# Optimization experiments

Measured on AMD Instinct MI355X. Metric: run time of the kernel, lower is better.

## Reference

```python
import jax, jax.numpy as jnp
import numpy as np

T_SCHEDULE = 999.0
LOG_2PI = float(np.log(2.0 * np.pi))


def setup_inputs() -> dict:
    key = jax.random.key(0)
    k1, k2, k3 = jax.random.split(key, 3)
    xt = jax.random.normal(k1, (128, 3, 32, 32), dtype=jnp.float32)
    # integer-style diffusion timesteps in [0, 900); divided by t_schedule=999 inside
    t = jax.random.uniform(k2, (128,), dtype=jnp.float32) * 900.0
    gt_images = jax.random.normal(k3, (20000, 3, 32, 32), dtype=jnp.float32)
    return {"xt": xt, "t": t, "gt_images": gt_images}


def reference(xt, t, gt_images):
    # AnalyticFlow.forward_fast
    B = xt.shape[0]
    N = gt_images.shape[0]
    x = jax.lax.stop_gradient(xt.reshape(B, -1))  # original detaches x
    gt = gt_images.reshape(N, -1)                 # [N, D]
    D = x.shape[-1]
    tt = t / T_SCHEDULE                           # [B]
    sig = 1.0 - tt                                # [B]
    # log N(term_2; 0, I) summed over D, where term_2 = (x - t*gt)/(1-t).
    # ||x - t*gt||^2 = ||x||^2 - 2 t x.gt + t^2 ||gt||^2  (avoids B*N*D tensor)
    x2 = jnp.sum(x * x, axis=-1)                  # [B]
    g2 = jnp.sum(gt * gt, axis=-1)                # [N]
    xg = x @ gt.T                                 # [B, N] GEMM
    sq = x2[:, None] - 2.0 * tt[:, None] * xg + (tt * tt)[:, None] * g2[None, :]
    log_p = -0.5 * sq / (sig * sig)[:, None] - 0.5 * D * LOG_2PI  # [B, N]
    log_p = log_p - jnp.max(log_p)                # global-max shift as in original
    eta = jax.nn.softmax(log_p, axis=1)           # [B, N], rows sum to 1
    # drift = mean_n (N*eta_n) * (gt_n - x)/(1-t) = (eta @ gt - x)/(1-t)
    drift = (eta @ gt - x) / sig[:, None]         # [B, D]
    return drift.reshape(xt.shape)
```

## Files before the change

kernel.cpp:

```cpp
#include <hip/hip_runtime.h>
#include <stdint.h>

#define B_SZ   128
#define D_SZ   3072
#define N_SZ   20000
#define NPAD   20480

typedef __attribute__((ext_vector_type(8))) short  short8;
typedef __attribute__((ext_vector_type(4))) float  f32x4;

__device__ __forceinline__ unsigned short f2bf(float f) {
    unsigned u = __float_as_uint(f);
    u += 0x7FFFu + ((u >> 16) & 1u);
    return (unsigned short)(u >> 16);
}
__device__ __forceinline__ float bf2f(unsigned short h) {
    return __uint_as_float(((unsigned)h) << 16);
}
__device__ __forceinline__ unsigned fkey_enc(float f) {
    unsigned b = __float_as_uint(f);
    return (b & 0x80000000u) ? ~b : (b | 0x80000000u);
}
__device__ __forceinline__ float fkey_dec(unsigned u) {
    return __uint_as_float((u & 0x80000000u) ? (u ^ 0x80000000u) : ~u);
}

__device__ __forceinline__ void gl_lds16(const void* g, void* l) {
    __builtin_amdgcn_global_load_lds(
        (const __attribute__((address_space(1))) void*)g,
        (__attribute__((address_space(3))) void*)l, 16, 0, 0);
}

__global__ __launch_bounds__(256) void zero_ws(float* __restrict__ p)
{
    p[blockIdx.x * 256 + threadIdx.x] = 0.f;
}

__global__ __launch_bounds__(256) void prep_x(const float* __restrict__ x,
                                              unsigned short* __restrict__ xhi,
                                              unsigned short* __restrict__ xlo)
{
    int i = blockIdx.x * 256 + threadIdx.x;
    float v = x[i];
    unsigned short h = f2bf(v);
    xhi[i] = h;
    xlo[i] = f2bf(v - bf2f(h));
}

__global__ __launch_bounds__(256) void scores_kernel(
        const float* __restrict__ gt,
        const unsigned short* __restrict__ xhi,
        const unsigned short* __restrict__ xlo,
        float* __restrict__ XG,
        float* __restrict__ G2)
{
    __shared__ __align__(16) unsigned short Xhi_t[128 * 32];
    __shared__ __align__(16) unsigned short Xlo_t[128 * 32];
    __shared__ __align__(16) unsigned short Ghi_t[64 * 32];
    __shared__ __align__(16) unsigned short Glo_t[64 * 32];

    const int tid   = threadIdx.x;
    const int kc    = blockIdx.x & 7;
    const int nt    = blockIdx.x >> 3;
    const int nbase = nt * 64;
    const int kcb   = kc * 384;

    const int lane = tid & 63;
    const int wave = tid >> 6;
    const int mh = wave & 1;
    const int nh = wave >> 1;
    const int lm = lane & 15;
    const int qd = lane >> 4;

    const int gn = tid >> 2;
    const int gq = tid & 3;
    const int ng0 = nbase + gn;
    int grow = ng0 > N_SZ - 1 ? N_SZ - 1 : ng0;
    const float* gp0 = gt + (size_t)grow * D_SZ + kcb + gq * 8;

    float g2acc = 0.0f;

    f32x4 acc[4][2];
    #pragma unroll
    for (int i = 0; i < 4; i++)
        #pragma unroll
        for (int j = 0; j < 2; j++)
            acc[i][j] = (f32x4){0.f, 0.f, 0.f, 0.f};

    for (int k0 = 0; k0 < 384; k0 += 32) {
        #pragma unroll
        for (int i = 0; i < 2; i++) {
            int o  = (i * 256 + tid) * 16;
            int r  = o >> 6;
            int ke = (o & 63) >> 1;
            gl_lds16(xhi + (size_t)r * D_SZ + kcb + k0 + ke, (char*)Xhi_t + o);
            gl_lds16(xlo + (size_t)r * D_SZ + kcb + k0 + ke, (char*)Xlo_t + o);
        }
        f32x4 v0 = *(const f32x4*)(gp0 + k0);
        f32x4 v1 = *(const f32x4*)(gp0 + k0 + 4);
        short8 h8, l8;
        #pragma unroll
        for (int j = 0; j < 4; j++) {
            float a = v0[j], b = v1[j];
            unsigned short ha = f2bf(a), hb = f2bf(b);
            h8[j]     = (short)ha;  h8[j + 4] = (short)hb;
            l8[j]     = (short)f2bf(a - bf2f(ha));
            l8[j + 4] = (short)f2bf(b - bf2f(hb));
            g2acc += a * a + b * b;
        }
        *(short8*)&Ghi_t[gn * 32 + gq * 8] = h8;
        *(short8*)&Glo_t[gn * 32 + gq * 8] = l8;

        __syncthreads();

        short8 bhi[2], blo[2];
        #pragma unroll
        for (int ni = 0; ni < 2; ni++) {
            int r = nh * 32 + ni * 16 + lm;
            bhi[ni] = *(short8*)&Ghi_t[r * 32 + qd * 8];
            blo[ni] = *(short8*)&Glo_t[r * 32 + qd * 8];
        }
        #pragma unroll
        for (int mi = 0; mi < 4; mi++) {
            int r = mh * 64 + mi * 16 + lm;
            short8 ahi = *(short8*)&Xhi_t[r * 32 + qd * 8];
            short8 alo = *(short8*)&Xlo_t[r * 32 + qd * 8];
            #pragma unroll
            for (int ni = 0; ni < 2; ni++) {
                acc[mi][ni] = __builtin_amdgcn_mfma_f32_16x16x32_bf16(ahi, bhi[ni], acc[mi][ni], 0, 0, 0);
                acc[mi][ni] = __builtin_amdgcn_mfma_f32_16x16x32_bf16(ahi, blo[ni], acc[mi][ni], 0, 0, 0);
                acc[mi][ni] = __builtin_amdgcn_mfma_f32_16x16x32_bf16(alo, bhi[ni], acc[mi][ni], 0, 0, 0);
            }
        }
        __syncthreads();
    }

    g2acc += __shfl_xor(g2acc, 1);
    g2acc += __shfl_xor(g2acc, 2);
    if (gq == 0 && ng0 < N_SZ) atomicAdd(&G2[ng0], g2acc);

    #pragma unroll
    for (int mi = 0; mi < 4; mi++) {
        #pragma unroll
        for (int ni = 0; ni < 2; ni++) {
            int ncol = nh * 32 + ni * 16 + lm;
            int ng = nbase + ncol;
            if (ng < N_SZ) {
                #pragma unroll
                for (int i = 0; i < 4; i++) {
                    int m = mh * 64 + mi * 16 + qd * 4 + i;
                    atomicAdd(&XG[(size_t)m * NPAD + ng], acc[mi][ni][i]);
                }
            }
        }
    }
}

__global__ __launch_bounds__(256) void maxk(
        const float* __restrict__ XG, const float* __restrict__ G2,
        const float* __restrict__ tarr, unsigned* __restrict__ Mkey)
{
    const int b  = blockIdx.x >> 3;
    const int ch = blockIdx.x & 7;
    const int tid = threadIdx.x;
    float tt  = tarr[b] / 999.0f;
    float sig = 1.0f - tt;
    float inv = 1.0f / (sig * sig);
    float c1 = tt * inv, c2 = 0.5f * tt * tt * inv;
    const float* xg = XG + (size_t)b * NPAD;
    __shared__ float wred[4];

    float mx = -3.402823466e+38f;
    int n0 = ch * 2560;
    for (int n = n0 + tid; n < n0 + 2560; n += 256)
        if (n < N_SZ) mx = fmaxf(mx, c1 * xg[n] - c2 * G2[n]);
    #pragma unroll
    for (int o = 32; o > 0; o >>= 1) mx = fmaxf(mx, __shfl_xor(mx, o));
    if ((tid & 63) == 0) wred[tid >> 6] = mx;
    __syncthreads();
    if (tid == 0) {
        mx = fmaxf(fmaxf(wred[0], wred[1]), fmaxf(wred[2], wred[3]));
        atomicMax(&Mkey[b], fkey_enc(mx));
    }
}

__global__ __launch_bounds__(256) void expk(
        const float* __restrict__ XG, const float* __restrict__ G2,
        const float* __restrict__ tarr, const unsigned* __restrict__ Mkey,
        unsigned short* __restrict__ P, float* __restrict__ L)
{
    const int b  = blockIdx.x >> 3;
    const int ch = blockIdx.x & 7;
    const int tid = threadIdx.x;
    float tt  = tarr[b] / 999.0f;
    float sig = 1.0f - tt;
    float inv = 1.0f / (sig * sig);
    float c1 = tt * inv, c2 = 0.5f * tt * tt * inv;
    float m = fkey_dec(Mkey[b]);
    const float* xg = XG + (size_t)b * NPAD;
    unsigned short* prow = P + (size_t)b * NPAD;
    __shared__ float wred[4];

    float sum = 0.f;
    int n0 = ch * 2560;
    for (int n = n0 + tid; n < n0 + 2560; n += 256) {
        float p = 0.f;
        if (n < N_SZ) { p = expf(c1 * xg[n] - c2 * G2[n] - m); sum += p; }
        prow[n] = f2bf(p);
    }
    #pragma unroll
    for (int o = 32; o > 0; o >>= 1) sum += __shfl_xor(sum, o);
    if ((tid & 63) == 0) wred[tid >> 6] = sum;
    __syncthreads();
    if (tid == 0) atomicAdd(&L[b], wred[0] + wred[1] + wred[2] + wred[3]);
}

__global__ __launch_bounds__(256) void drift_kernel(
        const float* __restrict__ gt,
        const unsigned short* __restrict__ P,
        float* __restrict__ Dacc)
{
    __shared__ __align__(16) unsigned short Pt[128 * 32];
    __shared__ __align__(16) unsigned short Gt[128 * 40];

    const int tid = threadIdx.x;
    const int nt = blockIdx.x % 24;
    const int kc = blockIdx.x / 24;
    const int dbase = nt * 128;

    const int lane = tid & 63;
    const int wave = tid >> 6;
    const int mh = wave & 1;
    const int dh = wave >> 1;
    const int lm = lane & 15;
    const int qd = lane >> 4;

    const int dg = tid & 31;
    const int kq = tid >> 5;

    f32x4 acc[4][4];
    #pragma unroll
    for (int i = 0; i < 4; i++)
        #pragma unroll
        for (int j = 0; j < 4; j++)
            acc[i][j] = (f32x4){0.f, 0.f, 0.f, 0.f};

    for (int s = 0; s < 16; s++) {
        int kb = kc * 512 + s * 32;
        #pragma unroll
        for (int i = 0; i < 2; i++) {
            int o  = (i * 256 + tid) * 16;
            int r  = o >> 6;
            int ke = (o & 63) >> 1;
            gl_lds16(P + (size_t)r * NPAD + kb + ke, (char*)Pt + o);
        }
        f32x4 row[4];
        #pragma unroll
        for (int i = 0; i < 4; i++) {
            int kg = kb + kq * 4 + i;
            if (kg > N_SZ - 1) kg = N_SZ - 1;
            row[i] = *(const f32x4*)(gt + (size_t)kg * D_SZ + dbase + dg * 4);
        }
        #pragma unroll
        for (int j = 0; j < 4; j++) {
            unsigned long long pk =
                  (unsigned long long)f2bf(row[0][j])
                | ((unsigned long long)f2bf(row[1][j]) << 16)
                | ((unsigned long long)f2bf(row[2][j]) << 32)
                | ((unsigned long long)f2bf(row[3][j]) << 48);
            *(unsigned long long*)((char*)Gt + (size_t)(dg * 4 + j) * 80 + kq * 8) = pk;
        }
        __syncthreads();

        short8 af[4], bf8[4];
        #pragma unroll
        for (int mi = 0; mi < 4; mi++)
            af[mi] = *(short8*)&Pt[(mh * 64 + mi * 16 + lm) * 32 + qd * 8];
        #pragma unroll
        for (int ni = 0; ni < 4; ni++)
            bf8[ni] = *(short8*)((char*)Gt + (size_t)(dh * 64 + ni * 16 + lm) * 80 + qd * 16);
        #pragma unroll
        for (int mi = 0; mi < 4; mi++)
            #pragma unroll
            for (int ni = 0; ni < 4; ni++)
                acc[mi][ni] = __builtin_amdgcn_mfma_f32_16x16x32_bf16(af[mi], bf8[ni], acc[mi][ni], 0, 0, 0);
        __syncthreads();
    }

    #pragma unroll
    for (int mi = 0; mi < 4; mi++)
        #pragma unroll
        for (int ni = 0; ni < 4; ni++) {
            int d = dbase + dh * 64 + ni * 16 + lm;
            #pragma unroll
            for (int i = 0; i < 4; i++) {
                int m = mh * 64 + mi * 16 + qd * 4 + i;
                atomicAdd(&Dacc[(size_t)m * D_SZ + d], acc[mi][ni][i]);
            }
        }
}

__global__ __launch_bounds__(256) void epilogue_kernel(
        const float* __restrict__ Dacc, const float* __restrict__ L,
        const float* __restrict__ x, const float* __restrict__ tarr,
        float* __restrict__ out)
{
    int i = blockIdx.x * 256 + threadIdx.x;
    int b = i / D_SZ;
    float tt = tarr[b] / 999.0f;
    float sig = 1.0f - tt;
    out[i] = (Dacc[i] / L[b] - x[i]) / sig;
}

extern "C" void kernel_launch(void* const* d_in, const int* in_sizes, int n_in,
                              void* d_out, int out_size, void* d_ws, size_t ws_size,
                              hipStream_t stream)
{
    const float* xt = (const float*)d_in[0];
    const float* t  = (const float*)d_in[1];
    const float* gt = (const float*)d_in[2];
    float* out = (float*)d_out;

    char* ws = (char*)d_ws;
    float*          XG  = (float*)         (ws + 0);
    float*          G2  = (float*)         (ws + 10485760);
    float*          Dacc= (float*)         (ws + 10567680);
    unsigned*       Mkey= (unsigned*)      (ws + 12140544);
    float*          L   = (float*)         (ws + 12141056);
    unsigned short* Xhi = (unsigned short*)(ws + 12141568);
    unsigned short* Xlo = (unsigned short*)(ws + 12928000);
    unsigned short* P   = (unsigned short*)(ws + 13714432);

    zero_ws       <<<11857, 256, 0, stream>>>((float*)ws);
    prep_x        <<< 1536, 256, 0, stream>>>(xt, Xhi, Xlo);
    scores_kernel <<< 2504, 256, 0, stream>>>(gt, Xhi, Xlo, XG, G2);
    maxk          <<< 1024, 256, 0, stream>>>(XG, G2, t, Mkey);
    expk          <<< 1024, 256, 0, stream>>>(XG, G2, t, Mkey, P, L);
    drift_kernel  <<<  960, 256, 0, stream>>>(gt, P, Dacc);
    epilogue_kernel<<<1536, 256, 0, stream>>>(Dacc, L, xt, t, out);
}
```

Before: 494.1 us.

## Load MFMA operands directly from global into registers, drop LDS staging in scores and drift

The scores kernel no longer stages X and G tiles through shared memory. Each lane loads its MFMA fragments straight from global memory, with register double-buffering (prefetch of the next k-step), and does the hi/lo bf16 split in registers using packed bf16 conversion intrinsics. The drift kernel likewise reads P fragments directly from global and uses packed conversions for the gt tile. This removes the LDS round trips and both barriers in the scores loop, and it sets a launch-bounds occupancy hint. The cost is redundant global loads across waves (each G row is reread by both mh halves and each X row by both nh halves) and more register pressure.

Result: slower. 602.3 us (+21.9%).

```diff
diff --git a/kernel.cpp b/kernel.cpp
--- a/kernel.cpp
+++ b/kernel.cpp
@@ -1,4 +1,5 @@
 #include <hip/hip_runtime.h>
+#include <hip/hip_bf16.h>
 #include <stdint.h>
 
 #define B_SZ   128
@@ -6,8 +7,10 @@
 #define N_SZ   20000
 #define NPAD   20480
 
-typedef __attribute__((ext_vector_type(8))) short  short8;
-typedef __attribute__((ext_vector_type(4))) float  f32x4;
+typedef __attribute__((ext_vector_type(8))) short        short8;
+typedef __attribute__((ext_vector_type(4))) float        f32x4;
+typedef __attribute__((ext_vector_type(4))) unsigned int uint4v;
+typedef __attribute__((ext_vector_type(2))) unsigned int uint2v;
 
 __device__ __forceinline__ unsigned short f2bf(float f) {
     unsigned u = __float_as_uint(f);
@@ -17,18 +20,18 @@
 __device__ __forceinline__ float bf2f(unsigned short h) {
     return __uint_as_float(((unsigned)h) << 16);
 }
+__device__ __forceinline__ unsigned pk2bf(float a, float b) {
+    __hip_bfloat162 h = __float22bfloat162_rn(make_float2(a, b));
+    unsigned r;
+    __builtin_memcpy(&r, &h, 4);
+    return r;
+}
 __device__ __forceinline__ unsigned fkey_enc(float f) {
     unsigned b = __float_as_uint(f);
     return (b & 0x80000000u) ? ~b : (b | 0x80000000u);
 }
 __device__ __forceinline__ float fkey_dec(unsigned u) {
     return __uint_as_float((u & 0x80000000u) ? (u ^ 0x80000000u) : ~u);
-}
-
-__device__ __forceinline__ void gl_lds16(const void* g, void* l) {
-    __builtin_amdgcn_global_load_lds(
-        (const __attribute__((address_space(1))) void*)g,
-        (__attribute__((address_space(3))) void*)l, 16, 0, 0);
 }
 
 __global__ __launch_bounds__(256) void zero_ws(float* __restrict__ p)
@@ -47,18 +50,13 @@
     xlo[i] = f2bf(v - bf2f(h));
 }
 
-__global__ __launch_bounds__(256) void scores_kernel(
+__global__ __launch_bounds__(256, 3) void scores_kernel(
         const float* __restrict__ gt,
         const unsigned short* __restrict__ xhi,
         const unsigned short* __restrict__ xlo,
         float* __restrict__ XG,
         float* __restrict__ G2)
 {
-    __shared__ __align__(16) unsigned short Xhi_t[128 * 32];
-    __shared__ __align__(16) unsigned short Xlo_t[128 * 32];
-    __shared__ __align__(16) unsigned short Ghi_t[64 * 32];
-    __shared__ __align__(16) unsigned short Glo_t[64 * 32];
-
     const int tid   = threadIdx.x;
     const int kc    = blockIdx.x & 7;
     const int nt    = blockIdx.x >> 3;
@@ -72,13 +70,23 @@
     const int lm = lane & 15;
     const int qd = lane >> 4;
 
-    const int gn = tid >> 2;
-    const int gq = tid & 3;
-    const int ng0 = nbase + gn;
-    int grow = ng0 > N_SZ - 1 ? N_SZ - 1 : ng0;
-    const float* gp0 = gt + (size_t)grow * D_SZ + kcb + gq * 8;
-
-    float g2acc = 0.0f;
+    int   nidx[2]; bool nval[2];
+    const float* gp[2];
+    #pragma unroll
+    for (int ni = 0; ni < 2; ni++) {
+        int n = nbase + nh * 32 + ni * 16 + lm;
+        nval[ni] = (n < N_SZ);
+        nidx[ni] = n;
+        int ncl = nval[ni] ? n : (N_SZ - 1);
+        gp[ni] = gt + (size_t)ncl * D_SZ + kcb + qd * 8;
+    }
+    const unsigned short *xph[4], *xpl[4];
+    #pragma unroll
+    for (int mi = 0; mi < 4; mi++) {
+        int m = mh * 64 + mi * 16 + lm;
+        xph[mi] = xhi + (size_t)m * D_SZ + kcb + qd * 8;
+        xpl[mi] = xlo + (size_t)m * D_SZ + kcb + qd * 8;
+    }
 
     f32x4 acc[4][2];
     #pragma unroll
@@ -86,66 +94,100 @@
         #pragma unroll
         for (int j = 0; j < 2; j++)
             acc[i][j] = (f32x4){0.f, 0.f, 0.f, 0.f};
-
-    for (int k0 = 0; k0 < 384; k0 += 32) {
-        #pragma unroll
-        for (int i = 0; i < 2; i++) {
-            int o  = (i * 256 + tid) * 16;
-            int r  = o >> 6;
-            int ke = (o & 63) >> 1;
-            gl_lds16(xhi + (size_t)r * D_SZ + kcb + k0 + ke, (char*)Xhi_t + o);
-            gl_lds16(xlo + (size_t)r * D_SZ + kcb + k0 + ke, (char*)Xlo_t + o);
-        }
-        f32x4 v0 = *(const f32x4*)(gp0 + k0);
-        f32x4 v1 = *(const f32x4*)(gp0 + k0 + 4);
-        short8 h8, l8;
-        #pragma unroll
-        for (int j = 0; j < 4; j++) {
-            float a = v0[j], b = v1[j];
-            unsigned short ha = f2bf(a), hb = f2bf(b);
-            h8[j]     = (short)ha;  h8[j + 4] = (short)hb;
-            l8[j]     = (short)f2bf(a - bf2f(ha));
-            l8[j + 4] = (short)f2bf(b - bf2f(hb));
-            g2acc += a * a + b * b;
-        }
-        *(short8*)&Ghi_t[gn * 32 + gq * 8] = h8;
-        *(short8*)&Glo_t[gn * 32 + gq * 8] = l8;
-
-        __syncthreads();
-
-        short8 bhi[2], blo[2];
+    float g2a[2] = {0.f, 0.f};
+
+    f32x4 gv[2][2];
+    short8 ah[4], al[4];
+    #pragma unroll
+    for (int ni = 0; ni < 2; ni++) {
+        gv[ni][0] = *(const f32x4*)(gp[ni]);
+        gv[ni][1] = *(const f32x4*)(gp[ni] + 4);
+    }
+    #pragma unroll
+    for (int mi = 0; mi < 4; mi++) {
+        ah[mi] = *(const short8*)(xph[mi]);
+        al[mi] = *(const short8*)(xpl[mi]);
+    }
+
+    #pragma unroll
+    for (int k = 0; k < 12; k++) {
+        f32x4 gvn[2][2];
+        short8 ahn[4], aln[4];
+        if (k < 11) {
+            const int ko = (k + 1) * 32;
+            #pragma unroll
+            for (int ni = 0; ni < 2; ni++) {
+                gvn[ni][0] = *(const f32x4*)(gp[ni] + ko);
+                gvn[ni][1] = *(const f32x4*)(gp[ni] + ko + 4);
+            }
+            #pragma unroll
+            for (int mi = 0; mi < 4; mi++) {
+                ahn[mi] = *(const short8*)(xph[mi] + ko);
+                aln[mi] = *(const short8*)(xpl[mi] + ko);
+            }
+        }
+
+        short8 bh[2], bl[2];
         #pragma unroll
         for (int ni = 0; ni < 2; ni++) {
-            int r = nh * 32 + ni * 16 + lm;
-            bhi[ni] = *(short8*)&Ghi_t[r * 32 + qd * 8];
-            blo[ni] = *(short8*)&Glo_t[r * 32 + qd * 8];
-        }
+            f32x4 v0 = gv[ni][0], v1 = gv[ni][1];
+            unsigned u0 = pk2bf(v0[0], v0[1]);
+            unsigned u1 = pk2bf(v0[2], v0[3]);
+            unsigned u2 = pk2bf(v1[0], v1[1]);
+            unsigned u3 = pk2bf(v1[2], v1[3]);
+            float r0 = v0[0] - __uint_as_float(u0 << 16);
+            float r1 = v0[1] - __uint_as_float(u0 & 0xFFFF0000u);
+            float r2 = v0[2] - __uint_as_float(u1 << 16);
+            float r3 = v0[3] - __uint_as_float(u1 & 0xFFFF0000u);
+            float r4 = v1[0] - __uint_as_float(u2 << 16);
+            float r5 = v1[1] - __uint_as_float(u2 & 0xFFFF0000u);
+            float r6 = v1[2] - __uint_as_float(u3 << 16);
+            float r7 = v1[3] - __uint_as_float(u3 & 0xFFFF0000u);
+            unsigned w0 = pk2bf(r0, r1);
+            unsigned w1 = pk2bf(r2, r3);
+            unsigned w2 = pk2bf(r4, r5);
+            unsigned w3 = pk2bf(r6, r7);
+            uint4v hv = (uint4v){u0, u1, u2, u3};
+            uint4v lv = (uint4v){w0, w1, w2, w3};
+            __builtin_memcpy(&bh[ni], &hv, 16);
+            __builtin_memcpy(&bl[ni], &lv, 16);
+            if (mh == 0) {
+                g2a[ni] += v0[0]*v0[0] + v0[1]*v0[1] + v0[2]*v0[2] + v0[3]*v0[3]
+                         + v1[0]*v1[0] + v1[1]*v1[1] + v1[2]*v1[2] + v1[3]*v1[3];
+            }
+        }
+
         #pragma unroll
         for (int mi = 0; mi < 4; mi++) {
-            int r = mh * 64 + mi * 16 + lm;
-            short8 ahi = *(short8*)&Xhi_t[r * 32 + qd * 8];
-            short8 alo = *(short8*)&Xlo_t[r * 32 + qd * 8];
             #pragma unroll
             for (int ni = 0; ni < 2; ni++) {
-                acc[mi][ni] = __builtin_amdgcn_mfma_f32_16x16x32_bf16(ahi, bhi[ni], acc[mi][ni], 0, 0, 0);
-                acc[mi][ni] = __builtin_amdgcn_mfma_f32_16x16x32_bf16(ahi, blo[ni], acc[mi][ni], 0, 0, 0);
-                acc[mi][ni] = __builtin_amdgcn_mfma_f32_16x16x32_bf16(alo, bhi[ni], acc[mi][ni], 0, 0, 0);
-            }
-        }
-        __syncthreads();
-    }
-
-    g2acc += __shfl_xor(g2acc, 1);
-    g2acc += __shfl_xor(g2acc, 2);
-    if (gq == 0 && ng0 < N_SZ) atomicAdd(&G2[ng0], g2acc);
+                acc[mi][ni] = __builtin_amdgcn_mfma_f32_16x16x32_bf16(ah[mi], bh[ni], acc[mi][ni], 0, 0, 0);
+                acc[mi][ni] = __builtin_amdgcn_mfma_f32_16x16x32_bf16(ah[mi], bl[ni], acc[mi][ni], 0, 0, 0);
+                acc[mi][ni] = __builtin_amdgcn_mfma_f32_16x16x32_bf16(al[mi], bh[ni], acc[mi][ni], 0, 0, 0);
+            }
+        }
+
+        if (k < 11) {
+            #pragma unroll
+            for (int ni = 0; ni < 2; ni++) { gv[ni][0] = gvn[ni][0]; gv[ni][1] = gvn[ni][1]; }
+            #pragma unroll
+            for (int mi = 0; mi < 4; mi++) { ah[mi] = ahn[mi]; al[mi] = aln[mi]; }
+        }
+    }
+
+    #pragma unroll
+    for (int ni = 0; ni < 2; ni++) {
+        g2a[ni] += __shfl_xor(g2a[ni], 16);
+        g2a[ni] += __shfl_xor(g2a[ni], 32);
+        if (mh == 0 && qd == 0 && nval[ni]) atomicAdd(&G2[nidx[ni]], g2a[ni]);
+    }
 
     #pragma unroll
     for (int mi = 0; mi < 4; mi++) {
         #pragma unroll
         for (int ni = 0; ni < 2; ni++) {
-            int ncol = nh * 32 + ni * 16 + lm;
-            int ng = nbase + ncol;
-            if (ng < N_SZ) {
+            int ng = nidx[ni];
+            if (nval[ni]) {
                 #pragma unroll
                 for (int i = 0; i < 4; i++) {
                     int m = mh * 64 + mi * 16 + qd * 4 + i;
@@ -220,7 +262,6 @@
         const unsigned short* __restrict__ P,
         float* __restrict__ Dacc)
 {
-    __shared__ __align__(16) unsigned short Pt[128 * 32];
     __shared__ __align__(16) unsigned short Gt[128 * 40];
 
     const int tid = threadIdx.x;
@@ -238,6 +279,11 @@
     const int dg = tid & 31;
     const int kq = tid >> 5;
 
+    const unsigned short* pp[4];
+    #pragma unroll
+    for (int mi = 0; mi < 4; mi++)
+        pp[mi] = P + (size_t)(mh * 64 + mi * 16 + lm) * NPAD + kc * 512 + qd * 8;
+
     f32x4 acc[4][4];
     #pragma unroll
     for (int i = 0; i < 4; i++)
@@ -247,13 +293,6 @@
 
     for (int s = 0; s < 16; s++) {
         int kb = kc * 512 + s * 32;
-        #pragma unroll
-        for (int i = 0; i < 2; i++) {
-            int o  = (i * 256 + tid) * 16;
-            int r  = o >> 6;
-            int ke = (o & 63) >> 1;
-            gl_lds16(P + (size_t)r * NPAD + kb + ke, (char*)Pt + o);
-        }
         f32x4 row[4];
         #pragma unroll
         for (int i = 0; i < 4; i++) {
@@ -263,19 +302,17 @@
         }
         #pragma unroll
         for (int j = 0; j < 4; j++) {
-            unsigned long long pk =
-                  (unsigned long long)f2bf(row[0][j])
-                | ((unsigned long long)f2bf(row[1][j]) << 16)
-                | ((unsigned long long)f2bf(row[2][j]) << 32)
-                | ((unsigned long long)f2bf(row[3][j]) << 48);
-            *(unsigned long long*)((char*)Gt + (size_t)(dg * 4 + j) * 80 + kq * 8) = pk;
+            unsigned u01 = pk2bf(row[0][j], row[1][j]);
+            unsigned u23 = pk2bf(row[2][j], row[3][j]);
+            uint2v pk = (uint2v){u01, u23};
+            __builtin_memcpy((char*)Gt + (size_t)(dg * 4 + j) * 80 + kq * 8, &pk, 8);
         }
         __syncthreads();
 
         short8 af[4], bf8[4];
         #pragma unroll
         for (int mi = 0; mi < 4; mi++)
-            af[mi] = *(short8*)&Pt[(mh * 64 + mi * 16 + lm) * 32 + qd * 8];
+            af[mi] = *(const short8*)(pp[mi] + s * 32);
         #pragma unroll
         for (int ni = 0; ni < 4; ni++)
             bf8[ni] = *(short8*)((char*)Gt + (size_t)(dh * 64 + ni * 16 + lm) * 80 + qd * 16);
```

## Replace split-K atomics with partial buffers and reduce passes, swizzle LDS tiles

Applied to the files above, without the earlier changes.

The score and drift GEMMs now write split-K partials to separate buffers with plain stores instead of float atomicAdd. A new sum8 kernel reduces the score partials, and the epilogue sums the 40 drift partials with vectorized loads. This removes atomic contention and most of the large workspace zeroing. LDS tiles get an XOR swizzle to cut bank conflicts, and bf16 packing uses the paired conversion intrinsic. The cost is much more workspace traffic: about 84 MB of score partials and 63 MB of drift partials written and then read back.

New measurement: 486.4 us. Within noise of the previous version (-1.6%).

```diff
diff --git a/kernel.cpp b/kernel.cpp
--- a/kernel.cpp
+++ b/kernel.cpp
@@ -1,13 +1,17 @@
 #include <hip/hip_runtime.h>
+#include <hip/hip_bf16.h>
 #include <stdint.h>
 
 #define B_SZ   128
 #define D_SZ   3072
 #define N_SZ   20000
 #define NPAD   20480
-
-typedef __attribute__((ext_vector_type(8))) short  short8;
-typedef __attribute__((ext_vector_type(4))) float  f32x4;
+#define BN     (B_SZ * NPAD)
+#define BD     (B_SZ * D_SZ)
+
+typedef __attribute__((ext_vector_type(8))) short        short8;
+typedef __attribute__((ext_vector_type(4))) float        f32x4;
+typedef __attribute__((ext_vector_type(2))) unsigned int uint2v;
 
 __device__ __forceinline__ unsigned short f2bf(float f) {
     unsigned u = __float_as_uint(f);
@@ -17,6 +21,12 @@
 __device__ __forceinline__ float bf2f(unsigned short h) {
     return __uint_as_float(((unsigned)h) << 16);
 }
+__device__ __forceinline__ unsigned pk2bf(float a, float b) {
+    __hip_bfloat162 h = __float22bfloat162_rn(make_float2(a, b));
+    unsigned r;
+    __builtin_memcpy(&r, &h, 4);
+    return r;
+}
 __device__ __forceinline__ unsigned fkey_enc(float f) {
     unsigned b = __float_as_uint(f);
     return (b & 0x80000000u) ? ~b : (b | 0x80000000u);
@@ -31,7 +41,9 @@
         (__attribute__((address_space(3))) void*)l, 16, 0, 0);
 }
 
-__global__ __launch_bounds__(256) void zero_ws(float* __restrict__ p)
+__device__ __forceinline__ int swz(int r, int q) { return q ^ ((r >> 1) & 3); }
+
+__global__ __launch_bounds__(256) void zero_small(float* __restrict__ p)
 {
     p[blockIdx.x * 256 + threadIdx.x] = 0.f;
 }
@@ -51,7 +63,7 @@
         const float* __restrict__ gt,
         const unsigned short* __restrict__ xhi,
         const unsigned short* __restrict__ xlo,
-        float* __restrict__ XG,
+        float* __restrict__ XG_part,
         float* __restrict__ G2)
 {
     __shared__ __align__(16) unsigned short Xhi_t[128 * 32];
@@ -77,6 +89,17 @@
     const int ng0 = nbase + gn;
     int grow = ng0 > N_SZ - 1 ? N_SZ - 1 : ng0;
     const float* gp0 = gt + (size_t)grow * D_SZ + kcb + gq * 8;
+    const int gwr = gn * 32 + swz(gn, gq) * 8;
+
+    int xsrc[2], xdst[2];
+    #pragma unroll
+    for (int i = 0; i < 2; i++) {
+        int o = (i * 256 + tid) * 16;
+        int r = o >> 6;
+        int j = (o >> 4) & 3;
+        xdst[i] = o;
+        xsrc[i] = r * D_SZ + kcb + swz(r, j) * 8;
+    }
 
     float g2acc = 0.0f;
 
@@ -90,11 +113,8 @@
     for (int k0 = 0; k0 < 384; k0 += 32) {
         #pragma unroll
         for (int i = 0; i < 2; i++) {
-            int o  = (i * 256 + tid) * 16;
-            int r  = o >> 6;
-            int ke = (o & 63) >> 1;
-            gl_lds16(xhi + (size_t)r * D_SZ + kcb + k0 + ke, (char*)Xhi_t + o);
-            gl_lds16(xlo + (size_t)r * D_SZ + kcb + k0 + ke, (char*)Xlo_t + o);
+            gl_lds16(xhi + xsrc[i] + k0, (char*)Xhi_t + xdst[i]);
+            gl_lds16(xlo + xsrc[i] + k0, (char*)Xlo_t + xdst[i]);
         }
         f32x4 v0 = *(const f32x4*)(gp0 + k0);
         f32x4 v1 = *(const f32x4*)(gp0 + k0 + 4);
@@ -108,8 +128,8 @@
             l8[j + 4] = (short)f2bf(b - bf2f(hb));
             g2acc += a * a + b * b;
         }
-        *(short8*)&Ghi_t[gn * 32 + gq * 8] = h8;
-        *(short8*)&Glo_t[gn * 32 + gq * 8] = l8;
+        *(short8*)&Ghi_t[gwr] = h8;
+        *(short8*)&Glo_t[gwr] = l8;
 
         __syncthreads();
 
@@ -117,14 +137,16 @@
         #pragma unroll
         for (int ni = 0; ni < 2; ni++) {
             int r = nh * 32 + ni * 16 + lm;
-            bhi[ni] = *(short8*)&Ghi_t[r * 32 + qd * 8];
-            blo[ni] = *(short8*)&Glo_t[r * 32 + qd * 8];
+            int sl = r * 32 + swz(r, qd) * 8;
+            bhi[ni] = *(short8*)&Ghi_t[sl];
+            blo[ni] = *(short8*)&Glo_t[sl];
         }
         #pragma unroll
         for (int mi = 0; mi < 4; mi++) {
             int r = mh * 64 + mi * 16 + lm;
-            short8 ahi = *(short8*)&Xhi_t[r * 32 + qd * 8];
-            short8 alo = *(short8*)&Xlo_t[r * 32 + qd * 8];
+            int sl = r * 32 + swz(r, qd) * 8;
+            short8 ahi = *(short8*)&Xhi_t[sl];
+            short8 alo = *(short8*)&Xlo_t[sl];
             #pragma unroll
             for (int ni = 0; ni < 2; ni++) {
                 acc[mi][ni] = __builtin_amdgcn_mfma_f32_16x16x32_bf16(ahi, bhi[ni], acc[mi][ni], 0, 0, 0);
@@ -139,6 +161,7 @@
     g2acc += __shfl_xor(g2acc, 2);
     if (gq == 0 && ng0 < N_SZ) atomicAdd(&G2[ng0], g2acc);
 
+    float* XGp = XG_part + (size_t)kc * BN;
     #pragma unroll
     for (int mi = 0; mi < 4; mi++) {
         #pragma unroll
@@ -149,11 +172,22 @@
                 #pragma unroll
                 for (int i = 0; i < 4; i++) {
                     int m = mh * 64 + mi * 16 + qd * 4 + i;
-                    atomicAdd(&XG[(size_t)m * NPAD + ng], acc[mi][ni][i]);
+                    XGp[(size_t)m * NPAD + ng] = acc[mi][ni][i];
                 }
             }
         }
     }
+}
+
+__global__ __launch_bounds__(256) void sum8(
+        const float* __restrict__ XG_part, float* __restrict__ XG)
+{
+    int i = (blockIdx.x * 256 + threadIdx.x) * 4;
+    f32x4 s = (f32x4){0.f, 0.f, 0.f, 0.f};
+    #pragma unroll
+    for (int kc = 0; kc < 8; kc++)
+        s += *(const f32x4*)(XG_part + (size_t)kc * BN + i);
+    *(f32x4*)(XG + i) = s;
 }
 
 __global__ __launch_bounds__(256) void maxk(
@@ -218,7 +252,7 @@
 __global__ __launch_bounds__(256) void drift_kernel(
         const float* __restrict__ gt,
         const unsigned short* __restrict__ P,
-        float* __restrict__ Dacc)
+        float* __restrict__ Dacc_part)
 {
     __shared__ __align__(16) unsigned short Pt[128 * 32];
     __shared__ __align__(16) unsigned short Gt[128 * 40];
@@ -238,6 +272,16 @@
     const int dg = tid & 31;
     const int kq = tid >> 5;
 
+    int psrc[2], pdst[2];
+    #pragma unroll
+    for (int i = 0; i < 2; i++) {
+        int o = (i * 256 + tid) * 16;
+        int r = o >> 6;
+        int j = (o >> 4) & 3;
+        pdst[i] = o;
+        psrc[i] = r * NPAD + kc * 512 + swz(r, j) * 8;
+    }
+
     f32x4 acc[4][4];
     #pragma unroll
     for (int i = 0; i < 4; i++)
@@ -248,12 +292,8 @@
     for (int s = 0; s < 16; s++) {
         int kb = kc * 512 + s * 32;
         #pragma unroll
-        for (int i = 0; i < 2; i++) {
-            int o  = (i * 256 + tid) * 16;
-            int r  = o >> 6;
-            int ke = (o & 63) >> 1;
-            gl_lds16(P + (size_t)r * NPAD + kb + ke, (char*)Pt + o);
-        }
+        for (int i = 0; i < 2; i++)
+            gl_lds16(P + psrc[i] + s * 32, (char*)Pt + pdst[i]);
         f32x4 row[4];
         #pragma unroll
         for (int i = 0; i < 4; i++) {
@@ -263,19 +303,19 @@
         }
         #pragma unroll
         for (int j = 0; j < 4; j++) {
-            unsigned long long pk =
-                  (unsigned long long)f2bf(row[0][j])
-                | ((unsigned long long)f2bf(row[1][j]) << 16)
-                | ((unsigned long long)f2bf(row[2][j]) << 32)
-                | ((unsigned long long)f2bf(row[3][j]) << 48);
-            *(unsigned long long*)((char*)Gt + (size_t)(dg * 4 + j) * 80 + kq * 8) = pk;
+            unsigned u01 = pk2bf(row[0][j], row[1][j]);
+            unsigned u23 = pk2bf(row[2][j], row[3][j]);
+            uint2v pk = (uint2v){u01, u23};
+            __builtin_memcpy((char*)Gt + (size_t)(dg * 4 + j) * 80 + kq * 8, &pk, 8);
         }
         __syncthreads();
 
         short8 af[4], bf8[4];
         #pragma unroll
-        for (int mi = 0; mi < 4; mi++)
-            af[mi] = *(short8*)&Pt[(mh * 64 + mi * 16 + lm) * 32 + qd * 8];
+        for (int mi = 0; mi < 4; mi++) {
+            int r = mh * 64 + mi * 16 + lm;
+            af[mi] = *(short8*)&Pt[r * 32 + swz(r, qd) * 8];
+        }
         #pragma unroll
         for (int ni = 0; ni < 4; ni++)
             bf8[ni] = *(short8*)((char*)Gt + (size_t)(dh * 64 + ni * 16 + lm) * 80 + qd * 16);
@@ -287,6 +327,7 @@
         __syncthreads();
     }
 
+    float* Dp = Dacc_part + (size_t)kc * BD;
     #pragma unroll
     for (int mi = 0; mi < 4; mi++)
         #pragma unroll
@@ -295,21 +336,30 @@
             #pragma unroll
             for (int i = 0; i < 4; i++) {
                 int m = mh * 64 + mi * 16 + qd * 4 + i;
-                atomicAdd(&Dacc[(size_t)m * D_SZ + d], acc[mi][ni][i]);
+                Dp[(size_t)m * D_SZ + d] = acc[mi][ni][i];
             }
         }
 }
 
 __global__ __launch_bounds__(256) void epilogue_kernel(
-        const float* __restrict__ Dacc, const float* __restrict__ L,
+        const float* __restrict__ Dacc_part, const float* __restrict__ L,
         const float* __restrict__ x, const float* __restrict__ tarr,
         float* __restrict__ out)
 {
-    int i = blockIdx.x * 256 + threadIdx.x;
+    int i = (blockIdx.x * 256 + threadIdx.x) * 4;
     int b = i / D_SZ;
+    f32x4 s = (f32x4){0.f, 0.f, 0.f, 0.f};
+    #pragma unroll
+    for (int kc = 0; kc < 40; kc++)
+        s += *(const f32x4*)(Dacc_part + (size_t)kc * BD + i);
     float tt = tarr[b] / 999.0f;
     float sig = 1.0f - tt;
-    out[i] = (Dacc[i] / L[b] - x[i]) / sig;
+    float invL = 1.0f / L[b];
+    f32x4 xv = *(const f32x4*)(x + i);
+    f32x4 o;
+    #pragma unroll
+    for (int j = 0; j < 4; j++) o[j] = (s[j] * invL - xv[j]) / sig;
+    *(f32x4*)(out + i) = o;
 }
 
 extern "C" void kernel_launch(void* const* d_in, const int* in_sizes, int n_in,
@@ -322,20 +372,22 @@
     float* out = (float*)d_out;
 
     char* ws = (char*)d_ws;
-    float*          XG  = (float*)         (ws + 0);
-    float*          G2  = (float*)         (ws + 10485760);
-    float*          Dacc= (float*)         (ws + 10567680);
-    unsigned*       Mkey= (unsigned*)      (ws + 12140544);
-    float*          L   = (float*)         (ws + 12141056);
-    unsigned short* Xhi = (unsigned short*)(ws + 12141568);
-    unsigned short* Xlo = (unsigned short*)(ws + 12928000);
-    unsigned short* P   = (unsigned short*)(ws + 13714432);
-
-    zero_ws       <<<11857, 256, 0, stream>>>((float*)ws);
+    float*          XG_part  = (float*)(ws + 0);
+    float*          XG       = (float*)(ws + 83886080);
+    float*          Dacc_part= (float*)(ws + 94371840);
+    float*          G2       = (float*)(ws + 157286400);
+    unsigned*       Mkey     = (unsigned*)(ws + 157368320);
+    float*          L        = (float*)(ws + 157368832);
+    unsigned short* Xhi      = (unsigned short*)(ws + 157369344);
+    unsigned short* Xlo      = (unsigned short*)(ws + 158155776);
+    unsigned short* P        = (unsigned short*)(ws + 158942208);
+
+    zero_small    <<<   81, 256, 0, stream>>>(G2);
     prep_x        <<< 1536, 256, 0, stream>>>(xt, Xhi, Xlo);
-    scores_kernel <<< 2504, 256, 0, stream>>>(gt, Xhi, Xlo, XG, G2);
+    scores_kernel <<< 2504, 256, 0, stream>>>(gt, Xhi, Xlo, XG_part, G2);
+    sum8          <<< 2560, 256, 0, stream>>>(XG_part, XG);
     maxk          <<< 1024, 256, 0, stream>>>(XG, G2, t, Mkey);
     expk          <<< 1024, 256, 0, stream>>>(XG, G2, t, Mkey, P, L);
-    drift_kernel  <<<  960, 256, 0, stream>>>(gt, P, Dacc);
-    epilogue_kernel<<<1536, 256, 0, stream>>>(Dacc, L, xt, t, out);
-}
+    drift_kernel  <<<  960, 256, 0, stream>>>(gt, P, Dacc_part);
+    epilogue_kernel<<< 384, 256, 0, stream>>>(Dacc_part, L, xt, t, out);
+}
```
